# Kernel tuning notes

Measured on AMD Instinct MI355X. Metric: run time of the kernel, lower is better.

## Reference

```python
import jax, jax.numpy as jnp
import numpy as np

B, L, V, D = 8, 2048, 1024, 512  # batch, seq (max_len), vocab_size (input feat), embedding_dim

def setup_inputs() -> dict:
    key = jax.random.key(0)
    kx, kq, kk, kv = jax.random.split(key, 4)
    scale = 1.0 / np.sqrt(V)
    return {
        "x": jax.random.normal(kx, (B, L, V), dtype=jnp.float32),
        "Wq": jax.random.uniform(kq, (D, V), dtype=jnp.float32, minval=-scale, maxval=scale),
        "Wk": jax.random.uniform(kk, (D, V), dtype=jnp.float32, minval=-scale, maxval=scale),
        "Wv": jax.random.uniform(kv, (D, V), dtype=jnp.float32, minval=-scale, maxval=scale),
    }

def reference(x, Wq, Wk, Wv):
    # nn.Linear without bias: y = x @ W.T
    q = jnp.einsum('blv,dv->bld', x, Wq)
    k = jnp.einsum('blv,dv->bld', x, Wk)
    v = jnp.einsum('blv,dv->bld', x, Wv)
    scores = jnp.einsum('bqd,bkd->bqk', q, k) / jnp.sqrt(jnp.float32(D))
    attn = jax.nn.softmax(scores, axis=2)
    return jnp.einsum('bqk,bkd->bqd', attn, v)
```

## Files before the change

### kernel.cpp

```cpp
#include <hip/hip_runtime.h>
#include <cstdint>
#include <cstddef>


typedef __attribute__((ext_vector_type(8))) __bf16 bf16x8;
typedef __attribute__((ext_vector_type(4))) float f32x4;
typedef __attribute__((ext_vector_type(4))) unsigned short ushort4v;
typedef __attribute__((ext_vector_type(4))) unsigned int uint4v;

__device__ __forceinline__ unsigned short f2bf(float f) {
  unsigned u = __float_as_uint(f);
  return (unsigned short)((u + 0x7fffu + ((u >> 16) & 1u)) >> 16);
}

__device__ __forceinline__ void async_load16(const unsigned short* g, unsigned short* l) {
  __builtin_amdgcn_global_load_lds(
      (__attribute__((address_space(1))) void*)(g),
      (__attribute__((address_space(3))) void*)(l), 16, 0, 0);
}

__global__ __launch_bounds__(256) void cvt_f32_bf16(const float* __restrict__ src,
                                                    unsigned short* __restrict__ dst) {
  int i = (blockIdx.x * 256 + threadIdx.x) * 4;
  float4 v = *(const float4*)(src + i);
  ushort4v o;
  o.x = f2bf(v.x); o.y = f2bf(v.y); o.z = f2bf(v.z); o.w = f2bf(v.w);
  *(ushort4v*)(dst + i) = o;
}

__global__ __launch_bounds__(256) void cvt_w3(const float* __restrict__ a,
                                              const float* __restrict__ b,
                                              const float* __restrict__ c,
                                              unsigned short* __restrict__ dst) {
  int bx = blockIdx.x;
  const float* src = (bx < 512) ? a : (bx < 1024) ? b : c;
  int seg = (bx < 512) ? 0 : (bx < 1024) ? 1 : 2;
  int i = ((bx & 511) * 256 + threadIdx.x) * 4;
  float4 v = *(const float4*)(src + i);
  ushort4v o;
  o.x = f2bf(v.x); o.y = f2bf(v.y); o.z = f2bf(v.z); o.w = f2bf(v.w);
  *(ushort4v*)(dst + seg * 524288 + i) = o;
}


__global__ __launch_bounds__(256) void gemm_qkv(
    const unsigned short* __restrict__ A0,
    const unsigned short* __restrict__ Bw,
    unsigned short* __restrict__ qk,
    unsigned short* __restrict__ vT) {
  __shared__ unsigned short sA[128 * 64];
  __shared__ unsigned short sB[128 * 64];
  const int tid = threadIdx.x;
  const int lane = tid & 63, wid = tid >> 6;
  const int wm = wid & 1, wn = wid >> 1;
  const int cl = lane & 15, g = lane >> 4;

  int flat = blockIdx.x + blockIdx.y * 12;
  int sub = flat >> 3;
  int bxp = sub % 12;
  int byp = (flat & 7) * 16 + sub / 12;

  const unsigned short* A = A0 + (size_t)byp * 128 * 1024;
  const unsigned short* B = Bw + (size_t)bxp * 128 * 1024;

  f32x4 acc[4][4] = {};

  for (int k0 = 0; k0 < 1024; k0 += 64) {
    __syncthreads();
    #pragma unroll
    for (int p = 0; p < 4; ++p) {
      int u = p * 256 + tid;
      int r = u >> 3, cs = (u & 7) ^ (r & 7);
      async_load16(&A[(size_t)r * 1024 + k0 + cs * 8], &sA[u * 8]);
      async_load16(&B[(size_t)r * 1024 + k0 + cs * 8], &sB[u * 8]);
    }
    __syncthreads();

    bf16x8 aF[4][2], bF[4][2];
    #pragma unroll
    for (int t = 0; t < 4; ++t)
      #pragma unroll
      for (int kh = 0; kh < 2; ++kh) {
        int ra = wm * 64 + t * 16 + cl;
        aF[t][kh] = *(const bf16x8*)&sA[(ra * 8 + ((kh * 4 + g) ^ (ra & 7))) * 8];
        int rb = wn * 64 + t * 16 + cl;
        bF[t][kh] = *(const bf16x8*)&sB[(rb * 8 + ((kh * 4 + g) ^ (rb & 7))) * 8];
      }
    #pragma unroll
    for (int mt = 0; mt < 4; ++mt)
      #pragma unroll
      for (int nt = 0; nt < 4; ++nt)
        #pragma unroll
        for (int kh = 0; kh < 2; ++kh)
          acc[mt][nt] = __builtin_amdgcn_mfma_f32_16x16x32_bf16(
              aF[mt][kh], bF[nt][kh], acc[mt][nt], 0, 0, 0);
  }

  if (bxp < 8) {
    unsigned short* Cc = qk + (size_t)byp * 128 * 1024 + (size_t)bxp * 128;
    #pragma unroll
    for (int mt = 0; mt < 4; ++mt)
      #pragma unroll
      for (int nt = 0; nt < 4; ++nt) {
        int col = wn * 64 + nt * 16 + cl;
        int row0 = wm * 64 + mt * 16 + g * 4;
        #pragma unroll
        for (int j = 0; j < 4; ++j)
          Cc[(size_t)(row0 + j) * 1024 + col] = f2bf(acc[mt][nt][j]);
      }
  } else {
    int nvx = bxp - 8;
    #pragma unroll
    for (int mt = 0; mt < 4; ++mt)
      #pragma unroll
      for (int nt = 0; nt < 4; ++nt) {
        int d = nvx * 128 + wn * 64 + nt * 16 + cl;
        int grow0 = byp * 128 + wm * 64 + mt * 16 + g * 4;
        int b = grow0 >> 11, l0 = grow0 & 2047;
        ushort4v o;
        o.x = f2bf(acc[mt][nt][0]); o.y = f2bf(acc[mt][nt][1]);
        o.z = f2bf(acc[mt][nt][2]); o.w = f2bf(acc[mt][nt][3]);
        *(ushort4v*)&vT[(size_t)b * 1048576 + (size_t)d * 2048 + l0] = o;
      }
  }
}

__global__ __launch_bounds__(256) void gemm_exp(
    const unsigned short* __restrict__ qk,
    unsigned short* __restrict__ S, float scale) {
  __shared__ unsigned short sA[128 * 64];
  __shared__ unsigned short sB[128 * 64];
  const int tid = threadIdx.x;
  const int lane = tid & 63, wid = tid >> 6;
  const int wm = wid & 1, wn = wid >> 1;
  const int cl = lane & 15, g = lane >> 4;

  int flat = blockIdx.x + (blockIdx.y << 4) + (blockIdx.z << 8);
  int z = flat & 7, rem = flat >> 3;
  int bxp = rem & 15, byp = rem >> 4;

  const unsigned short* A  = qk + (size_t)z * 2097152 + (size_t)byp * 128 * 1024;
  const unsigned short* Bk = qk + 512 + (size_t)z * 2097152 + (size_t)bxp * 128 * 1024;

  f32x4 acc[4][4] = {};

  for (int k0 = 0; k0 < 512; k0 += 64) {
    __syncthreads();
    #pragma unroll
    for (int p = 0; p < 4; ++p) {
      int u = p * 256 + tid;
      int r = u >> 3, cs = (u & 7) ^ (r & 7);
      async_load16(&A[(size_t)r * 1024 + k0 + cs * 8], &sA[u * 8]);
      async_load16(&Bk[(size_t)r * 1024 + k0 + cs * 8], &sB[u * 8]);
    }
    __syncthreads();

    bf16x8 aF[4][2], bF[4][2];
    #pragma unroll
    for (int t = 0; t < 4; ++t)
      #pragma unroll
      for (int kh = 0; kh < 2; ++kh) {
        int ra = wm * 64 + t * 16 + cl;
        aF[t][kh] = *(const bf16x8*)&sA[(ra * 8 + ((kh * 4 + g) ^ (ra & 7))) * 8];
        int rb = wn * 64 + t * 16 + cl;
        bF[t][kh] = *(const bf16x8*)&sB[(rb * 8 + ((kh * 4 + g) ^ (rb & 7))) * 8];
      }
    #pragma unroll
    for (int mt = 0; mt < 4; ++mt)
      #pragma unroll
      for (int nt = 0; nt < 4; ++nt)
        #pragma unroll
        for (int kh = 0; kh < 2; ++kh)
          acc[mt][nt] = __builtin_amdgcn_mfma_f32_16x16x32_bf16(
              aF[mt][kh], bF[nt][kh], acc[mt][nt], 0, 0, 0);
  }

  unsigned short* Cc = S + (size_t)z * 4194304 +
                       (size_t)byp * 128 * 2048 + (size_t)bxp * 128;
  #pragma unroll
  for (int mt = 0; mt < 4; ++mt)
    #pragma unroll
    for (int nt = 0; nt < 4; ++nt) {
      int col = wn * 64 + nt * 16 + cl;
      int row0 = wm * 64 + mt * 16 + g * 4;
      #pragma unroll
      for (int j = 0; j < 4; ++j)
        Cc[(size_t)(row0 + j) * 2048 + col] =
            f2bf(__expf(acc[mt][nt][j] * scale));
    }
}

__global__ __launch_bounds__(256) void gemm_pv(
    const unsigned short* __restrict__ P, const unsigned short* __restrict__ vT,
    float* __restrict__ out) {
  __shared__ unsigned short sA[128 * 64];
  __shared__ unsigned short sB[128 * 64];
  __shared__ float rs[128];
  const int tid = threadIdx.x;
  const int lane = tid & 63, wid = tid >> 6;
  const int wm = wid & 1, wn = wid >> 1;
  const int cl = lane & 15, g = lane >> 4;

  int flat = blockIdx.x + (blockIdx.y << 2) + (blockIdx.z << 6);
  int z = flat & 7, rem = flat >> 3;
  int bxp = rem & 3, byp = rem >> 2;

  const int m0 = byp * 128, n0 = bxp * 128;
  const unsigned short* A  = P + (size_t)z * 4194304 + (size_t)m0 * 2048;
  const unsigned short* Bv = vT + (size_t)z * 1048576 + (size_t)n0 * 2048;

  f32x4 acc[4][4] = {};
  float rsum[4] = {0.f, 0.f, 0.f, 0.f};

  for (int k0 = 0; k0 < 2048; k0 += 64) {
    __syncthreads();
    #pragma unroll
    for (int p = 0; p < 4; ++p) {
      int u = p * 256 + tid;
      int r = u >> 3, cs = (u & 7) ^ (r & 7);
      async_load16(&A[(size_t)r * 2048 + k0 + cs * 8], &sA[u * 8]);
      async_load16(&Bv[(size_t)r * 2048 + k0 + cs * 8], &sB[u * 8]);
    }
    __syncthreads();

    bf16x8 aF[4][2], bF[4][2];
    #pragma unroll
    for (int t = 0; t < 4; ++t)
      #pragma unroll
      for (int kh = 0; kh < 2; ++kh) {
        int ra = wm * 64 + t * 16 + cl;
        aF[t][kh] = *(const bf16x8*)&sA[(ra * 8 + ((kh * 4 + g) ^ (ra & 7))) * 8];
        int rb = wn * 64 + t * 16 + cl;
        bF[t][kh] = *(const bf16x8*)&sB[(rb * 8 + ((kh * 4 + g) ^ (rb & 7))) * 8];
      }
    #pragma unroll
    for (int t = 0; t < 4; ++t)
      #pragma unroll
      for (int kh = 0; kh < 2; ++kh) {
        uint4v u = __builtin_bit_cast(uint4v, aF[t][kh]);
        #pragma unroll
        for (int q = 0; q < 4; ++q)
          rsum[t] += __uint_as_float(u[q] << 16) +
                     __uint_as_float(u[q] & 0xffff0000u);
      }
    #pragma unroll
    for (int mt = 0; mt < 4; ++mt)
      #pragma unroll
      for (int nt = 0; nt < 4; ++nt)
        #pragma unroll
        for (int kh = 0; kh < 2; ++kh)
          acc[mt][nt] = __builtin_amdgcn_mfma_f32_16x16x32_bf16(
              aF[mt][kh], bF[nt][kh], acc[mt][nt], 0, 0, 0);
  }

  #pragma unroll
  for (int mt = 0; mt < 4; ++mt) {
    float v = rsum[mt];
    v += __shfl_xor(v, 16, 64);
    v += __shfl_xor(v, 32, 64);
    if (wn == 0 && lane < 16) rs[wm * 64 + mt * 16 + lane] = v;
  }
  __syncthreads();

  #pragma unroll
  for (int mt = 0; mt < 4; ++mt) {
    int row0l = wm * 64 + mt * 16 + g * 4;
    float inv[4];
    #pragma unroll
    for (int j = 0; j < 4; ++j) inv[j] = __builtin_amdgcn_rcpf(rs[row0l + j]);
    #pragma unroll
    for (int nt = 0; nt < 4; ++nt) {
      int col = n0 + wn * 64 + nt * 16 + cl;
      float* op = out + ((size_t)z * 2048 + m0 + row0l) * 512 + col;
      #pragma unroll
      for (int j = 0; j < 4; ++j)
        op[(size_t)j * 512] = acc[mt][nt][j] * inv[j];
    }
  }
}

extern "C" void kernel_launch(void* const* d_in, const int* in_sizes, int n_in,
                              void* d_out, int out_size, void* d_ws, size_t ws_size,
                              hipStream_t stream) {
  const float* x  = (const float*)d_in[0];
  const float* Wq = (const float*)d_in[1];
  const float* Wk = (const float*)d_in[2];
  const float* Wv = (const float*)d_in[3];
  float* out = (float*)d_out;
  char* ws = (char*)d_ws;

  unsigned short* xb = (unsigned short*)ws;
  unsigned short* S  = (unsigned short*)ws;
  unsigned short* wf = (unsigned short*)(ws + 33554432);
  unsigned short* qk = (unsigned short*)(ws + 67108864);
  unsigned short* vT = (unsigned short*)(ws + 100663296);

  const float rsqrtD = 0.044194173824159216f;

  hipLaunchKernelGGL(cvt_f32_bf16, dim3(16384), dim3(256), 0, stream, x, xb);
  hipLaunchKernelGGL(cvt_w3, dim3(1536), dim3(256), 0, stream, Wq, Wk, Wv, wf);

  hipLaunchKernelGGL(gemm_qkv, dim3(12, 128, 1), dim3(256), 0, stream, xb, wf, qk, vT);

  hipLaunchKernelGGL(gemm_exp, dim3(16, 16, 8), dim3(256), 0, stream, qk, S, rsqrtD);

  hipLaunchKernelGGL(gemm_pv, dim3(4, 16, 8), dim3(256), 0, stream, S, vT, out);

  (void)in_sizes; (void)n_in; (void)out_size; (void)ws_size;
}
```

Before: 262.3 us.

## Use triple-buffered 8-wave pipelined GEMM core for QKV and PV kernels

Adds a shared GEMM core that runs 512 threads on 256x128 tiles. It streams K-slices into three rotating LDS buffers with async global-to-LDS loads, waits with explicit vmcnt and raises priority around the MFMA bursts. This is meant to hide global load latency behind matrix math. The PV stage is transposed to compute out^T tiles, so row sums come from the B operand and results leave as float4 stores. The two conversion kernels are merged into one launch. The cost is 144 KB of dynamic LDS per block, which limits a CU to one block, and more reliance on hand-tuned waitcnt and barrier ordering.

New measurement: 268.3 us. +2.3%, slower.

```diff
diff --git a/kernel.cpp b/kernel.cpp
--- a/kernel.cpp
+++ b/kernel.cpp
@@ -19,85 +19,145 @@
       (__attribute__((address_space(3))) void*)(l), 16, 0, 0);
 }
 
-__global__ __launch_bounds__(256) void cvt_f32_bf16(const float* __restrict__ src,
-                                                    unsigned short* __restrict__ dst) {
-  int i = (blockIdx.x * 256 + threadIdx.x) * 4;
+__global__ __launch_bounds__(256) void cvt_all(
+    const float* __restrict__ x, const float* __restrict__ Wq,
+    const float* __restrict__ Wk, const float* __restrict__ Wv,
+    unsigned short* __restrict__ xb, unsigned short* __restrict__ wf) {
+  int u0 = blockIdx.x, tid = threadIdx.x;
+  const float* src;
+  unsigned short* dst;
+  int i;
+  if (u0 < 16384) {
+    i = (u0 * 256 + tid) * 4;
+    src = x; dst = xb;
+  } else {
+    int bx = u0 - 16384;
+    src = (bx < 512) ? Wq : (bx < 1024) ? Wk : Wv;
+    int seg = (bx < 512) ? 0 : (bx < 1024) ? 1 : 2;
+    i = ((bx & 511) * 256 + tid) * 4;
+    dst = wf + seg * 524288;
+  }
   float4 v = *(const float4*)(src + i);
   ushort4v o;
   o.x = f2bf(v.x); o.y = f2bf(v.y); o.z = f2bf(v.z); o.w = f2bf(v.w);
   *(ushort4v*)(dst + i) = o;
 }
 
-__global__ __launch_bounds__(256) void cvt_w3(const float* __restrict__ a,
-                                              const float* __restrict__ b,
-                                              const float* __restrict__ c,
-                                              unsigned short* __restrict__ dst) {
-  int bx = blockIdx.x;
-  const float* src = (bx < 512) ? a : (bx < 1024) ? b : c;
-  int seg = (bx < 512) ? 0 : (bx < 1024) ? 1 : 2;
-  int i = ((bx & 511) * 256 + threadIdx.x) * 4;
-  float4 v = *(const float4*)(src + i);
-  ushort4v o;
-  o.x = f2bf(v.x); o.y = f2bf(v.y); o.z = f2bf(v.z); o.w = f2bf(v.w);
-  *(ushort4v*)(dst + seg * 524288 + i) = o;
-}
-
-
-__global__ __launch_bounds__(256) void gemm_qkv(
+template <int NT, bool RSUM>
+__device__ __forceinline__ void core8p(
+    const unsigned short* __restrict__ A, const unsigned short* __restrict__ B,
+    int ldA, int ldB, unsigned short* smem, int tid,
+    f32x4 (&acc)[4][4], float (&rsum)[4]) {
+  const int lane = tid & 63, wid = tid >> 6;
+  const int wm = wid & 3, wn = wid >> 2;
+  const int cl = lane & 15, g = lane >> 4;
+  const int r0 = tid >> 3;
+  const int cs8 = ((tid & 7) ^ (r0 & 7)) * 8;
+
+  #pragma unroll
+  for (int p = 0; p < 4; ++p)
+    async_load16(&A[(size_t)(p * 64 + r0) * ldA + cs8], &smem[(p * 512 + tid) * 8]);
+  #pragma unroll
+  for (int p = 0; p < 2; ++p)
+    async_load16(&B[(size_t)(p * 64 + r0) * ldB + cs8], &smem[16384 + (p * 512 + tid) * 8]);
+  #pragma unroll
+  for (int p = 0; p < 4; ++p)
+    async_load16(&A[(size_t)(p * 64 + r0) * ldA + 64 + cs8], &smem[24576 + (p * 512 + tid) * 8]);
+  #pragma unroll
+  for (int p = 0; p < 2; ++p)
+    async_load16(&B[(size_t)(p * 64 + r0) * ldB + 64 + cs8], &smem[40960 + (p * 512 + tid) * 8]);
+  asm volatile("s_waitcnt vmcnt(6)" ::: "memory");
+  __builtin_amdgcn_s_barrier();
+
+  int cur = 0;
+  for (int t = 0; t < NT; ++t) {
+    unsigned short* bufc = smem + cur * 24576;
+    int nb = cur + 2; if (nb >= 3) nb -= 3;
+    unsigned short* bufn = smem + nb * 24576;
+    const bool st = (t + 2 < NT);
+    const int k2 = (t + 2) * 64;
+
+    #pragma unroll
+    for (int kh = 0; kh < 2; ++kh) {
+      bf16x8 a4[4], b4[4];
+      #pragma unroll
+      for (int mt = 0; mt < 4; ++mt) {
+        int rr = wm * 64 + mt * 16 + cl;
+        a4[mt] = *(const bf16x8*)&bufc[(rr * 8 + ((kh * 4 + g) ^ (rr & 7))) * 8];
+      }
+      #pragma unroll
+      for (int nt = 0; nt < 4; ++nt) {
+        int rr = wn * 64 + nt * 16 + cl;
+        b4[nt] = *(const bf16x8*)&bufc[16384 + (rr * 8 + ((kh * 4 + g) ^ (rr & 7))) * 8];
+      }
+      if (kh == 0) {
+        if (st) {
+          #pragma unroll
+          for (int p = 0; p < 4; ++p)
+            async_load16(&A[(size_t)(p * 64 + r0) * ldA + k2 + cs8],
+                         &bufn[(p * 512 + tid) * 8]);
+        }
+      } else {
+        if (st) {
+          #pragma unroll
+          for (int p = 0; p < 2; ++p)
+            async_load16(&B[(size_t)(p * 64 + r0) * ldB + k2 + cs8],
+                         &bufn[16384 + (p * 512 + tid) * 8]);
+          asm volatile("s_waitcnt vmcnt(6)" ::: "memory");
+        } else if (t + 1 < NT) {
+          asm volatile("s_waitcnt vmcnt(0)" ::: "memory");
+        }
+      }
+      __builtin_amdgcn_s_barrier();
+      asm volatile("s_waitcnt lgkmcnt(0)" ::: "memory");
+      __builtin_amdgcn_sched_barrier(0);
+      if (RSUM) {
+        #pragma unroll
+        for (int nt = 0; nt < 4; ++nt) {
+          uint4v u = __builtin_bit_cast(uint4v, b4[nt]);
+          #pragma unroll
+          for (int q = 0; q < 4; ++q)
+            rsum[nt] += __uint_as_float(u[q] << 16) +
+                        __uint_as_float(u[q] & 0xffff0000u);
+        }
+      }
+      __builtin_amdgcn_s_setprio(1);
+      #pragma unroll
+      for (int mt = 0; mt < 4; ++mt)
+        #pragma unroll
+        for (int nt = 0; nt < 4; ++nt)
+          acc[mt][nt] = __builtin_amdgcn_mfma_f32_16x16x32_bf16(
+              a4[mt], b4[nt], acc[mt][nt], 0, 0, 0);
+      __builtin_amdgcn_s_setprio(0);
+      __builtin_amdgcn_s_barrier();
+    }
+    cur = cur + 1; if (cur == 3) cur = 0;
+  }
+}
+
+__global__ __launch_bounds__(512, 2) void gemm_qkv8(
     const unsigned short* __restrict__ A0,
     const unsigned short* __restrict__ Bw,
     unsigned short* __restrict__ qk,
     unsigned short* __restrict__ vT) {
-  __shared__ unsigned short sA[128 * 64];
-  __shared__ unsigned short sB[128 * 64];
+  extern __shared__ __align__(16) unsigned short smem[];
   const int tid = threadIdx.x;
-  const int lane = tid & 63, wid = tid >> 6;
-  const int wm = wid & 1, wn = wid >> 1;
-  const int cl = lane & 15, g = lane >> 4;
-
-  int flat = blockIdx.x + blockIdx.y * 12;
+  int flat = blockIdx.x;
   int sub = flat >> 3;
   int bxp = sub % 12;
-  int byp = (flat & 7) * 16 + sub / 12;
-
-  const unsigned short* A = A0 + (size_t)byp * 128 * 1024;
+  int byp = (flat & 7) * 8 + sub / 12;
+  const unsigned short* A = A0 + (size_t)byp * 256 * 1024;
   const unsigned short* B = Bw + (size_t)bxp * 128 * 1024;
 
   f32x4 acc[4][4] = {};
-
-  for (int k0 = 0; k0 < 1024; k0 += 64) {
-    __syncthreads();
-    #pragma unroll
-    for (int p = 0; p < 4; ++p) {
-      int u = p * 256 + tid;
-      int r = u >> 3, cs = (u & 7) ^ (r & 7);
-      async_load16(&A[(size_t)r * 1024 + k0 + cs * 8], &sA[u * 8]);
-      async_load16(&B[(size_t)r * 1024 + k0 + cs * 8], &sB[u * 8]);
-    }
-    __syncthreads();
-
-    bf16x8 aF[4][2], bF[4][2];
-    #pragma unroll
-    for (int t = 0; t < 4; ++t)
-      #pragma unroll
-      for (int kh = 0; kh < 2; ++kh) {
-        int ra = wm * 64 + t * 16 + cl;
-        aF[t][kh] = *(const bf16x8*)&sA[(ra * 8 + ((kh * 4 + g) ^ (ra & 7))) * 8];
-        int rb = wn * 64 + t * 16 + cl;
-        bF[t][kh] = *(const bf16x8*)&sB[(rb * 8 + ((kh * 4 + g) ^ (rb & 7))) * 8];
-      }
-    #pragma unroll
-    for (int mt = 0; mt < 4; ++mt)
-      #pragma unroll
-      for (int nt = 0; nt < 4; ++nt)
-        #pragma unroll
-        for (int kh = 0; kh < 2; ++kh)
-          acc[mt][nt] = __builtin_amdgcn_mfma_f32_16x16x32_bf16(
-              aF[mt][kh], bF[nt][kh], acc[mt][nt], 0, 0, 0);
-  }
+  float rsum[4];
+  core8p<16, false>(A, B, 1024, 1024, smem, tid, acc, rsum);
+
+  const int lane = tid & 63, wid = tid >> 6;
+  const int wm = wid & 3, wn = wid >> 2, cl = lane & 15, g = lane >> 4;
 
   if (bxp < 8) {
-    unsigned short* Cc = qk + (size_t)byp * 128 * 1024 + (size_t)bxp * 128;
+    unsigned short* Cc = qk + (size_t)byp * 256 * 1024 + (size_t)bxp * 128;
     #pragma unroll
     for (int mt = 0; mt < 4; ++mt)
       #pragma unroll
@@ -115,7 +175,7 @@
       #pragma unroll
       for (int nt = 0; nt < 4; ++nt) {
         int d = nvx * 128 + wn * 64 + nt * 16 + cl;
-        int grow0 = byp * 128 + wm * 64 + mt * 16 + g * 4;
+        int grow0 = byp * 256 + wm * 64 + mt * 16 + g * 4;
         int b = grow0 >> 11, l0 = grow0 & 2047;
         ushort4v o;
         o.x = f2bf(acc[mt][nt][0]); o.y = f2bf(acc[mt][nt][1]);
@@ -125,9 +185,54 @@
   }
 }
 
+__global__ __launch_bounds__(512, 2) void gemm_pvT8(
+    const unsigned short* __restrict__ S, const unsigned short* __restrict__ vT,
+    float* __restrict__ out) {
+  extern __shared__ __align__(16) unsigned short smem[];
+  const int tid = threadIdx.x;
+  int flat = blockIdx.x;
+  int b = flat & 7, rem = flat >> 3;
+  int dblk = rem & 1, qblk = rem >> 1;
+  const unsigned short* A  = vT + (size_t)b * 1048576 + (size_t)dblk * 256 * 2048;
+  const unsigned short* Bs = S  + (size_t)b * 4194304 + (size_t)qblk * 128 * 2048;
+
+  f32x4 acc[4][4] = {};
+  float rsum[4] = {0.f, 0.f, 0.f, 0.f};
+  core8p<32, true>(A, Bs, 2048, 2048, smem, tid, acc, rsum);
+
+  const int lane = tid & 63, wid = tid >> 6;
+  const int wm = wid & 3, wn = wid >> 2, cl = lane & 15, g = lane >> 4;
+
+  #pragma unroll
+  for (int nt = 0; nt < 4; ++nt) {
+    float v = rsum[nt];
+    v += __shfl_xor(v, 16, 64);
+    v += __shfl_xor(v, 32, 64);
+    rsum[nt] = v;
+  }
+
+  #pragma unroll
+  for (int nt = 0; nt < 4; ++nt) {
+    float inv = __builtin_amdgcn_rcpf(rsum[nt]);
+    int qpos = qblk * 128 + wn * 64 + nt * 16 + cl;
+    #pragma unroll
+    for (int mt = 0; mt < 4; ++mt) {
+      int d0 = dblk * 256 + wm * 64 + mt * 16 + g * 4;
+      float* op = out + ((size_t)b * 2048 + qpos) * 512 + d0;
+      float4 o;
+      o.x = acc[mt][nt][0] * inv;
+      o.y = acc[mt][nt][1] * inv;
+      o.z = acc[mt][nt][2] * inv;
+      o.w = acc[mt][nt][3] * inv;
+      *(float4*)op = o;
+    }
+  }
+}
+
 __global__ __launch_bounds__(256) void gemm_exp(
     const unsigned short* __restrict__ qk,
-    unsigned short* __restrict__ S, float scale) {
+    unsigned short* __restrict__ S) {
+  const float scale = 0.044194173824159216f;
   __shared__ unsigned short sA[128 * 64];
   __shared__ unsigned short sB[128 * 64];
   const int tid = threadIdx.x;
@@ -188,95 +293,6 @@
         Cc[(size_t)(row0 + j) * 2048 + col] =
             f2bf(__expf(acc[mt][nt][j] * scale));
     }
-}
-
-__global__ __launch_bounds__(256) void gemm_pv(
-    const unsigned short* __restrict__ P, const unsigned short* __restrict__ vT,
-    float* __restrict__ out) {
-  __shared__ unsigned short sA[128 * 64];
-  __shared__ unsigned short sB[128 * 64];
-  __shared__ float rs[128];
-  const int tid = threadIdx.x;
-  const int lane = tid & 63, wid = tid >> 6;
-  const int wm = wid & 1, wn = wid >> 1;
-  const int cl = lane & 15, g = lane >> 4;
-
-  int flat = blockIdx.x + (blockIdx.y << 2) + (blockIdx.z << 6);
-  int z = flat & 7, rem = flat >> 3;
-  int bxp = rem & 3, byp = rem >> 2;
-
-  const int m0 = byp * 128, n0 = bxp * 128;
-  const unsigned short* A  = P + (size_t)z * 4194304 + (size_t)m0 * 2048;
-  const unsigned short* Bv = vT + (size_t)z * 1048576 + (size_t)n0 * 2048;
-
-  f32x4 acc[4][4] = {};
-  float rsum[4] = {0.f, 0.f, 0.f, 0.f};
-
-  for (int k0 = 0; k0 < 2048; k0 += 64) {
-    __syncthreads();
-    #pragma unroll
-    for (int p = 0; p < 4; ++p) {
-      int u = p * 256 + tid;
-      int r = u >> 3, cs = (u & 7) ^ (r & 7);
-      async_load16(&A[(size_t)r * 2048 + k0 + cs * 8], &sA[u * 8]);
-      async_load16(&Bv[(size_t)r * 2048 + k0 + cs * 8], &sB[u * 8]);
-    }
-    __syncthreads();
-
-    bf16x8 aF[4][2], bF[4][2];
-    #pragma unroll
-    for (int t = 0; t < 4; ++t)
-      #pragma unroll
-      for (int kh = 0; kh < 2; ++kh) {
-        int ra = wm * 64 + t * 16 + cl;
-        aF[t][kh] = *(const bf16x8*)&sA[(ra * 8 + ((kh * 4 + g) ^ (ra & 7))) * 8];
-        int rb = wn * 64 + t * 16 + cl;
-        bF[t][kh] = *(const bf16x8*)&sB[(rb * 8 + ((kh * 4 + g) ^ (rb & 7))) * 8];
-      }
-    #pragma unroll
-    for (int t = 0; t < 4; ++t)
-      #pragma unroll
-      for (int kh = 0; kh < 2; ++kh) {
-        uint4v u = __builtin_bit_cast(uint4v, aF[t][kh]);
-        #pragma unroll
-        for (int q = 0; q < 4; ++q)
-          rsum[t] += __uint_as_float(u[q] << 16) +
-                     __uint_as_float(u[q] & 0xffff0000u);
-      }
-    #pragma unroll
-    for (int mt = 0; mt < 4; ++mt)
-      #pragma unroll
-      for (int nt = 0; nt < 4; ++nt)
-        #pragma unroll
-        for (int kh = 0; kh < 2; ++kh)
-          acc[mt][nt] = __builtin_amdgcn_mfma_f32_16x16x32_bf16(
-              aF[mt][kh], bF[nt][kh], acc[mt][nt], 0, 0, 0);
-  }
-
-  #pragma unroll
-  for (int mt = 0; mt < 4; ++mt) {
-    float v = rsum[mt];
-    v += __shfl_xor(v, 16, 64);
-    v += __shfl_xor(v, 32, 64);
-    if (wn == 0 && lane < 16) rs[wm * 64 + mt * 16 + lane] = v;
-  }
-  __syncthreads();
-
-  #pragma unroll
-  for (int mt = 0; mt < 4; ++mt) {
-    int row0l = wm * 64 + mt * 16 + g * 4;
-    float inv[4];
-    #pragma unroll
-    for (int j = 0; j < 4; ++j) inv[j] = __builtin_amdgcn_rcpf(rs[row0l + j]);
-    #pragma unroll
-    for (int nt = 0; nt < 4; ++nt) {
-      int col = n0 + wn * 64 + nt * 16 + cl;
-      float* op = out + ((size_t)z * 2048 + m0 + row0l) * 512 + col;
-      #pragma unroll
-      for (int j = 0; j < 4; ++j)
-        op[(size_t)j * 512] = acc[mt][nt][j] * inv[j];
-    }
-  }
 }
 
 extern "C" void kernel_launch(void* const* d_in, const int* in_sizes, int n_in,
@@ -295,16 +311,25 @@
   unsigned short* qk = (unsigned short*)(ws + 67108864);
   unsigned short* vT = (unsigned short*)(ws + 100663296);
 
-  const float rsqrtD = 0.044194173824159216f;
-
-  hipLaunchKernelGGL(cvt_f32_bf16, dim3(16384), dim3(256), 0, stream, x, xb);
-  hipLaunchKernelGGL(cvt_w3, dim3(1536), dim3(256), 0, stream, Wq, Wk, Wv, wf);
-
-  hipLaunchKernelGGL(gemm_qkv, dim3(12, 128, 1), dim3(256), 0, stream, xb, wf, qk, vT);
-
-  hipLaunchKernelGGL(gemm_exp, dim3(16, 16, 8), dim3(256), 0, stream, qk, S, rsqrtD);
-
-  hipLaunchKernelGGL(gemm_pv, dim3(4, 16, 8), dim3(256), 0, stream, S, vT, out);
+  static bool inited = false;
+  if (!inited) {
+    hipFuncSetAttribute((const void*)gemm_qkv8,
+                        hipFuncAttributeMaxDynamicSharedMemorySize, 147456);
+    hipFuncSetAttribute((const void*)gemm_pvT8,
+                        hipFuncAttributeMaxDynamicSharedMemorySize, 147456);
+    inited = true;
+  }
+
+  hipLaunchKernelGGL(cvt_all, dim3(17920), dim3(256), 0, stream,
+                     x, Wq, Wk, Wv, xb, wf);
+
+  hipLaunchKernelGGL(gemm_qkv8, dim3(768), dim3(512), 147456, stream,
+                     xb, wf, qk, vT);
+
+  hipLaunchKernelGGL(gemm_exp, dim3(16, 16, 8), dim3(256), 0, stream, qk, S);
+
+  hipLaunchKernelGGL(gemm_pvT8, dim3(256), dim3(512), 147456, stream,
+                     S, vT, out);
 
   (void)in_sizes; (void)n_in; (void)out_size; (void)ws_size;
 }
```
